# Kernel optimization log

Measured on AMD Instinct MI355X. Metric: run time of the kernel, lower is better.

The kernel has to match this reference:

```python
import jax, jax.numpy as jnp
import numpy as np

NH = 8
D_MODEL = 512
D_K = D_MODEL // NH
B, S = 2, 4096


def setup_inputs() -> dict:
    key = jax.random.key(0)
    ks = jax.random.split(key, 8)
    scale = 1.0 / np.sqrt(D_MODEL)
    return {
        "query": jax.random.normal(ks[0], (B, S, D_MODEL), dtype=jnp.float32),
        "key": jax.random.normal(ks[1], (B, S, D_MODEL), dtype=jnp.float32),
        "value": jax.random.normal(ks[2], (B, S, D_MODEL), dtype=jnp.float32),
        "mask": jax.random.randint(ks[3], (B, 1, S, S), 0, 2) > 0,
        "Wq": jax.random.normal(ks[4], (D_MODEL, D_MODEL), dtype=jnp.float32) * scale,
        "Wk": jax.random.normal(ks[5], (D_MODEL, D_MODEL), dtype=jnp.float32) * scale,
        "Wv": jax.random.normal(ks[6], (D_MODEL, D_MODEL), dtype=jnp.float32) * scale,
        "Wo": jax.random.normal(ks[7], (D_MODEL, D_MODEL), dtype=jnp.float32) * scale,
    }


def reference(query, key, value, mask, Wq, Wk, Wv, Wo):
    # Linear (no bias): torch Linear stores W as [out, in], y = x @ W^T.
    def proj(x, W):
        # [B, S, D] -> [B, nh, S, d_k]
        y = jnp.einsum("bsd,ed->bse", x, W)
        return y.reshape(B, S, NH, D_K).transpose(0, 2, 1, 3)

    q = proj(query, Wq)
    k = proj(key, Wk)
    v = proj(value, Wv)

    scores = jnp.einsum("bhqd,bhkd->bhqk", q, k) / jnp.sqrt(jnp.float32(D_K))
    scores = jnp.where(mask, jnp.float32(-1e9), scores)
    p_attn = jax.nn.softmax(scores, axis=-1)
    x = jnp.einsum("bhqk,bhkd->bhqd", p_attn, v)  # [B, nh, S, d_k]
    x = x.transpose(0, 2, 1, 3).reshape(B, S, D_MODEL)
    return jnp.einsum("bsd,ed->bse", x, Wo)
```

## Files before the change

kernel.cpp:

```cpp
#include <hip/hip_runtime.h>


#define S_LEN   4096
#define DM      512
#define NHEAD   8
#define DKH     64
#define NEG_BIG (-1e9f)
#define MINIT   (-3.402823466e38f)

typedef __bf16 bf16x8 __attribute__((ext_vector_type(8)));
typedef __bf16 bf16x4 __attribute__((ext_vector_type(4)));
typedef float  f32x4  __attribute__((ext_vector_type(4)));
typedef unsigned long long u64;

__device__ inline uint4 cvt8(float4 a, float4 b) {
    union { bf16x8 v; uint4 u; } c;
    c.v[0] = (__bf16)a.x; c.v[1] = (__bf16)a.y;
    c.v[2] = (__bf16)a.z; c.v[3] = (__bf16)a.w;
    c.v[4] = (__bf16)b.x; c.v[5] = (__bf16)b.y;
    c.v[6] = (__bf16)b.z; c.v[7] = (__bf16)b.w;
    return c.u;
}

__global__ __launch_bounds__(256)
void pack_mask(const int* __restrict__ m, u64* __restrict__ bits)
{
    const size_t i = (size_t)blockIdx.x * 256 + threadIdx.x;
    const u64 b = __ballot(m[i] != 0);
    if ((threadIdx.x & 63) == 0) bits[i >> 6] = b;
}

template<int MODE>
__global__ __launch_bounds__(512, 4)
void gemm_bf16(const void* __restrict__ Xv0, const void* __restrict__ Xv1,
               const void* __restrict__ Xv2,
               const float* __restrict__ W0, const float* __restrict__ W1,
               const float* __restrict__ W2,
               void* __restrict__ Yv0, void* __restrict__ Yv1,
               void* __restrict__ Yv2)
{
    const void* Xv; const float* W; void* Yv;
    if (blockIdx.z == 0)      { Xv = Xv0; W = W0; Yv = Yv0; }
    else if (blockIdx.z == 1) { Xv = Xv1; W = W1; Yv = Yv1; }
    else                      { Xv = Xv2; W = W2; Yv = Yv2; }
    const float oscale = (MODE == 0 && blockIdx.z == 0) ? 0.125f : 1.0f;

    __shared__ __align__(16) char lds[32768];
    char* Xs = lds;
    char* Ws = lds + 16384;

    const int tid  = threadIdx.x;
    const int lane = tid & 63;
    const int l15  = lane & 15;
    const int lhi  = lane >> 4;
    const int w    = tid >> 6;
    const int wr   = w >> 2;
    const int wc   = w & 3;
    const int row0 = blockIdx.x << 7;
    const int col0 = blockIdx.y << 7;

    const int sr = tid >> 2;
    const int sc = (tid & 3) << 1;

    f32x4 acc[4][2];
    #pragma unroll
    for (int m = 0; m < 4; ++m)
        #pragma unroll
        for (int n = 0; n < 2; ++n)
            acc[m][n] = (f32x4){0.f, 0.f, 0.f, 0.f};

    for (int k0 = 0; k0 < DM; k0 += 64) {
        uint4 xa, xb, wa, wb;
        if (MODE == 0) {
            const float* X = (const float*)Xv;
            const size_t base = (size_t)(row0 + sr) * DM + k0 + sc * 8;
            const float4 x0 = *(const float4*)&X[base];
            const float4 x1 = *(const float4*)&X[base + 4];
            const float4 x2 = *(const float4*)&X[base + 8];
            const float4 x3 = *(const float4*)&X[base + 12];
            xa = cvt8(x0, x1); xb = cvt8(x2, x3);
        } else {
            const __bf16* X = (const __bf16*)Xv;
            const size_t base = (size_t)(row0 + sr) * DM + k0 + sc * 8;
            xa = *(const uint4*)&X[base];
            xb = *(const uint4*)&X[base + 8];
        }
        {
            const size_t base = (size_t)(col0 + sr) * DM + k0 + sc * 8;
            const float4 w0_ = *(const float4*)&W[base];
            const float4 w1_ = *(const float4*)&W[base + 4];
            const float4 w2_ = *(const float4*)&W[base + 8];
            const float4 w3_ = *(const float4*)&W[base + 12];
            wa = cvt8(w0_, w1_); wb = cvt8(w2_, w3_);
        }
        __syncthreads();
        *(uint4*)(Xs + sr * 128 + ((sc       ^ (sr & 7)) << 4)) = xa;
        *(uint4*)(Xs + sr * 128 + (((sc + 1) ^ (sr & 7)) << 4)) = xb;
        *(uint4*)(Ws + sr * 128 + ((sc       ^ (sr & 7)) << 4)) = wa;
        *(uint4*)(Ws + sr * 128 + (((sc + 1) ^ (sr & 7)) << 4)) = wb;
        __syncthreads();

        #pragma unroll
        for (int kk = 0; kk < 2; ++kk) {
            bf16x8 af[4], bfr[2];
            #pragma unroll
            for (int m = 0; m < 4; ++m) {
                const int r = wr * 64 + m * 16 + l15;
                af[m] = *(const bf16x8*)(Xs + r * 128 + ((((kk << 2) + lhi) ^ (r & 7)) << 4));
            }
            #pragma unroll
            for (int n = 0; n < 2; ++n) {
                const int r = wc * 32 + n * 16 + l15;
                bfr[n] = *(const bf16x8*)(Ws + r * 128 + ((((kk << 2) + lhi) ^ (r & 7)) << 4));
            }
            #pragma unroll
            for (int m = 0; m < 4; ++m)
                #pragma unroll
                for (int n = 0; n < 2; ++n)
                    acc[m][n] = __builtin_amdgcn_mfma_f32_16x16x32_bf16(af[m], bfr[n], acc[m][n], 0, 0, 0);
        }
    }

    #pragma unroll
    for (int m = 0; m < 4; ++m) {
        #pragma unroll
        for (int n = 0; n < 2; ++n) {
            #pragma unroll
            for (int r = 0; r < 4; ++r) {
                const int row = row0 + wr * 64 + m * 16 + lhi * 4 + r;
                const int col = col0 + wc * 32 + n * 16 + l15;
                if (MODE == 0) {
                    const int b = row >> 12, srow = row & 4095;
                    const int h = col >> 6,  dk = col & 63;
                    ((__bf16*)Yv)[(((size_t)(b * NHEAD + h)) * S_LEN + srow) * DKH + dk] =
                        (__bf16)(acc[m][n][r] * oscale);
                } else {
                    ((float*)Yv)[(size_t)row * DM + col] = acc[m][n][r];
                }
            }
        }
    }
}

__global__ __launch_bounds__(512, 4)
void attn_mfma(const __bf16* __restrict__ Q, const __bf16* __restrict__ K,
               const __bf16* __restrict__ V, const u64* __restrict__ bits,
               __bf16* __restrict__ ctx)
{
    __shared__ __align__(16) char lds[32768];
    char* Ks = lds;
    char* Vt = lds + 8192;
    char* Ps = lds + 16384;

    const int tid  = threadIdx.x;
    const int lane = tid & 63;
    const int w    = tid >> 6;
    const int l15  = lane & 15;
    const int lhi  = lane >> 4;
    const int q0   = blockIdx.x << 7;
    const int h    = blockIdx.y;
    const int b    = blockIdx.z;

    const __bf16* Qb = Q + (size_t)(b * NHEAD + h) * S_LEN * DKH;
    const __bf16* Kb = K + (size_t)(b * NHEAD + h) * S_LEN * DKH;
    const __bf16* Vb = V + (size_t)(b * NHEAD + h) * S_LEN * DKH;

    const int qrow = q0 + w * 16 + l15;
    const u64* Mb = bits + (size_t)b * (S_LEN * (S_LEN / 64)) + (size_t)qrow * 64;

    const bf16x8 qa0 = *(const bf16x8*)&Qb[(size_t)qrow * DKH + lhi * 8];
    const bf16x8 qa1 = *(const bf16x8*)&Qb[(size_t)qrow * DKH + 32 + lhi * 8];

    char* psb = Ps + w * 2048;

    f32x4 o[4];
    float m_r = MINIT, l_r = 0.f;
    #pragma unroll
    for (int dt = 0; dt < 4; ++dt) o[dt] = (f32x4){0.f, 0.f, 0.f, 0.f};

    const int kj   = tid >> 3;
    const int kseg = tid & 7;
    const int vj   = tid & 63;
    const int vd0  = (tid >> 6) * 8;

    for (int kt = 0; kt < S_LEN / 64; ++kt) {
        const int j0 = kt << 6;
        const uint4 kreg = *(const uint4*)&Kb[(size_t)(j0 + kj) * DKH + kseg * 8];
        const uint4 vreg = *(const uint4*)&Vb[(size_t)(j0 + vj) * DKH + vd0];
        const u64   mw   = Mb[kt];

        __syncthreads();
        *(uint4*)(Ks + kj * 128 + ((kseg ^ (kj & 7)) << 4)) = kreg;
        {
            const __bf16* vr = (const __bf16*)&vreg;
            #pragma unroll
            for (int i = 0; i < 8; ++i) {
                const int d = vd0 + i;
                int off = d * 128 + vj * 2;
                off ^= (d & 7) << 4;
                *(__bf16*)(Vt + off) = vr[i];
            }
        }
        __syncthreads();

        f32x4 s[4];
        #pragma unroll
        for (int t = 0; t < 4; ++t) {
            const int krow = t * 16 + l15;
            const int off = krow * 128 + ((lhi ^ (krow & 7)) << 4);
            const bf16x8 kb0 = *(const bf16x8*)(Ks + off);
            const bf16x8 kb1 = *(const bf16x8*)(Ks + (off ^ 64));
            f32x4 z = (f32x4){0.f, 0.f, 0.f, 0.f};
            z = __builtin_amdgcn_mfma_f32_16x16x32_bf16(kb0, qa0, z, 0, 0, 0);
            s[t] = __builtin_amdgcn_mfma_f32_16x16x32_bf16(kb1, qa1, z, 0, 0, 0);
        }

        const unsigned int lo = (unsigned int)mw, hi = (unsigned int)(mw >> 32);
        unsigned int shf[4];
        shf[0] = lo >> (lhi << 2);
        shf[1] = lo >> (16 + (lhi << 2));
        shf[2] = hi >> (lhi << 2);
        shf[3] = hi >> (16 + (lhi << 2));

        float pv[4][4];
        #pragma unroll
        for (int t = 0; t < 4; ++t)
            #pragma unroll
            for (int r = 0; r < 4; ++r)
                pv[t][r] = ((shf[t] >> r) & 1) ? NEG_BIG : s[t][r];

        float tmax = pv[0][0];
        #pragma unroll
        for (int t = 0; t < 4; ++t)
            #pragma unroll
            for (int r = 0; r < 4; ++r)
                tmax = fmaxf(tmax, pv[t][r]);
        tmax = fmaxf(tmax, __shfl_xor(tmax, 16));
        tmax = fmaxf(tmax, __shfl_xor(tmax, 32));

        if (!__all(tmax <= m_r + 8.f)) {
            const float newm  = fmaxf(m_r, tmax);
            const float alpha = __expf(m_r - newm);
            m_r = newm;
            l_r *= alpha;
            #pragma unroll
            for (int dt = 0; dt < 4; ++dt) {
                o[dt][0] *= alpha; o[dt][1] *= alpha;
                o[dt][2] *= alpha; o[dt][3] *= alpha;
            }
        }

        float rsum = 0.f;
        #pragma unroll
        for (int t = 0; t < 4; ++t)
            #pragma unroll
            for (int r = 0; r < 4; ++r) {
                pv[t][r] = __expf(pv[t][r] - m_r);
                rsum += pv[t][r];
            }
        rsum += __shfl_xor(rsum, 16);
        rsum += __shfl_xor(rsum, 32);
        l_r += rsum;

        #pragma unroll
        for (int t = 0; t < 4; ++t)
            #pragma unroll
            for (int c = 0; c < 2; ++c) {
                union { __bf16 h2[2]; unsigned int u; } pk;
                pk.h2[0] = (__bf16)pv[t][2 * c];
                pk.h2[1] = (__bf16)pv[t][2 * c + 1];
                const int kbyte = t * 32 + (lhi << 3) + (c << 2);
                const int off = l15 * 128
                              + (((kbyte >> 4) ^ (l15 & 7)) << 4) + (kbyte & 15);
                *(unsigned int*)(psb + off) = pk.u;
            }
        const int poff = l15 * 128 + ((lhi ^ (l15 & 7)) << 4);
        const bf16x8 pb0 = *(const bf16x8*)(psb + poff);
        const bf16x8 pb1 = *(const bf16x8*)(psb + (poff ^ 64));

        #pragma unroll
        for (int dt = 0; dt < 4; ++dt) {
            const int vrow = dt * 16 + l15;
            const int voff = vrow * 128 + ((lhi ^ (vrow & 7)) << 4);
            const bf16x8 vb0 = *(const bf16x8*)(Vt + voff);
            const bf16x8 vb1 = *(const bf16x8*)(Vt + (voff ^ 64));
            o[dt] = __builtin_amdgcn_mfma_f32_16x16x32_bf16(vb0, pb0, o[dt], 0, 0, 0);
            o[dt] = __builtin_amdgcn_mfma_f32_16x16x32_bf16(vb1, pb1, o[dt], 0, 0, 0);
        }
    }

    const float inv = 1.f / l_r;
    #pragma unroll
    for (int dt = 0; dt < 4; ++dt) {
        bf16x4 ov;
        ov[0] = (__bf16)(o[dt][0] * inv);
        ov[1] = (__bf16)(o[dt][1] * inv);
        ov[2] = (__bf16)(o[dt][2] * inv);
        ov[3] = (__bf16)(o[dt][3] * inv);
        *(bf16x4*)&ctx[((size_t)b * S_LEN + qrow) * DM + h * DKH + dt * 16 + lhi * 4] = ov;
    }
}

extern "C" void kernel_launch(void* const* d_in, const int* in_sizes, int n_in,
                              void* d_out, int out_size, void* d_ws, size_t ws_size,
                              hipStream_t stream)
{
    const float* q    = (const float*)d_in[0];
    const float* k    = (const float*)d_in[1];
    const float* v    = (const float*)d_in[2];
    const int*   mask = (const int*)d_in[3];
    const float* Wq   = (const float*)d_in[4];
    const float* Wk   = (const float*)d_in[5];
    const float* Wv   = (const float*)d_in[6];
    const float* Wo   = (const float*)d_in[7];
    float* out = (float*)d_out;

    const size_t per = (size_t)2 * S_LEN * DM;
    __bf16* Qh  = (__bf16*)d_ws;
    __bf16* Kh  = Qh + per;
    __bf16* Vh  = Kh + per;
    __bf16* ctx = Vh + per;
    u64*    bits = (u64*)(ctx + per);

    pack_mask<<<dim3((2 * S_LEN * S_LEN) / 256), dim3(256), 0, stream>>>(mask, bits);

    gemm_bf16<0><<<dim3(64, 4, 3), dim3(512), 0, stream>>>(
        q, k, v, Wq, Wk, Wv, Qh, Kh, Vh);

    attn_mfma<<<dim3(S_LEN / 128, NHEAD, 2), dim3(512), 0, stream>>>(
        Qh, Kh, Vh, bits, ctx);

    gemm_bf16<1><<<dim3(64, 4, 1), dim3(512), 0, stream>>>(
        ctx, ctx, ctx, Wo, Wo, Wo, out, out, out);
}
```

Measured before the change: 436.6 us.

## Pre-cast weights, use direct-to-LDS loads, double-buffer attention K/V tiles

A new kernel casts all four weight matrices to bf16 once per call. The GEMMs then stream W, and the bf16 ctx input in the output projection, straight into LDS with global_load_lds. Epilogue stores are vectorized by swapping the MFMA operands so each lane holds contiguous columns. The attention kernel double-buffers K/V tiles in a larger LDS allocation, prefetching the next tile during compute, keeping one barrier per iteration and raising wave priority around the MFMA sections. This trades an extra small launch and higher LDS use, which may reduce occupancy, for overlap of loads with compute.

```diff
diff --git a/kernel.cpp b/kernel.cpp
--- a/kernel.cpp
+++ b/kernel.cpp
@@ -5,6 +5,7 @@
 #define DM      512
 #define NHEAD   8
 #define DKH     64
+#define NT      (S_LEN / 64)
 #define NEG_BIG (-1e9f)
 #define MINIT   (-3.402823466e38f)
 
@@ -12,6 +13,12 @@
 typedef __bf16 bf16x4 __attribute__((ext_vector_type(4)));
 typedef float  f32x4  __attribute__((ext_vector_type(4)));
 typedef unsigned long long u64;
+
+__device__ inline void gload_lds16(const void* g, void* l) {
+    __builtin_amdgcn_global_load_lds(
+        (const __attribute__((address_space(1))) unsigned int*)g,
+        (__attribute__((address_space(3))) unsigned int*)l, 16, 0, 0);
+}
 
 __device__ inline uint4 cvt8(float4 a, float4 b) {
     union { bf16x8 v; uint4 u; } c;
@@ -23,6 +30,21 @@
 }
 
 __global__ __launch_bounds__(256)
+void cast_w(const float* __restrict__ Wq, const float* __restrict__ Wk,
+            const float* __restrict__ Wv, const float* __restrict__ Wo,
+            __bf16* __restrict__ out)
+{
+    const int t = blockIdx.x * 256 + threadIdx.x;
+    const int e = t * 8;
+    const int z = e >> 18;
+    const int i = e & 262143;
+    const float* W = (z == 0) ? Wq : (z == 1) ? Wk : (z == 2) ? Wv : Wo;
+    const float4 a = *(const float4*)&W[i];
+    const float4 b = *(const float4*)&W[i + 4];
+    *(uint4*)&out[e] = cvt8(a, b);
+}
+
+__global__ __launch_bounds__(256)
 void pack_mask(const int* __restrict__ m, u64* __restrict__ bits)
 {
     const size_t i = (size_t)blockIdx.x * 256 + threadIdx.x;
@@ -32,19 +54,12 @@
 
 template<int MODE>
 __global__ __launch_bounds__(512, 4)
-void gemm_bf16(const void* __restrict__ Xv0, const void* __restrict__ Xv1,
-               const void* __restrict__ Xv2,
-               const float* __restrict__ W0, const float* __restrict__ W1,
-               const float* __restrict__ W2,
-               void* __restrict__ Yv0, void* __restrict__ Yv1,
-               void* __restrict__ Yv2)
-{
-    const void* Xv; const float* W; void* Yv;
-    if (blockIdx.z == 0)      { Xv = Xv0; W = W0; Yv = Yv0; }
-    else if (blockIdx.z == 1) { Xv = Xv1; W = W1; Yv = Yv1; }
-    else                      { Xv = Xv2; W = W2; Yv = Yv2; }
-    const float oscale = (MODE == 0 && blockIdx.z == 0) ? 0.125f : 1.0f;
-
+void gemm_mfma(const float* __restrict__ X0, const float* __restrict__ X1,
+               const float* __restrict__ X2, const __bf16* __restrict__ Xb,
+               const __bf16* __restrict__ Wb,
+               __bf16* __restrict__ Y0, __bf16* __restrict__ Y1,
+               __bf16* __restrict__ Y2, float* __restrict__ Yf)
+{
     __shared__ __align__(16) char lds[32768];
     char* Xs = lds;
     char* Ws = lds + 16384;
@@ -58,6 +73,11 @@
     const int wc   = w & 3;
     const int row0 = blockIdx.x << 7;
     const int col0 = blockIdx.y << 7;
+    const int z    = blockIdx.z;
+
+    const float*  Xf = (z == 0) ? X0 : (z == 1) ? X1 : X2;
+    __bf16*       Yb = (z == 0) ? Y0 : (z == 1) ? Y1 : Y2;
+    const __bf16* W  = Wb + (size_t)(MODE == 0 ? z : 0) * DM * DM;
 
     const int sr = tid >> 2;
     const int sc = (tid & 3) << 1;
@@ -70,73 +90,76 @@
             acc[m][n] = (f32x4){0.f, 0.f, 0.f, 0.f};
 
     for (int k0 = 0; k0 < DM; k0 += 64) {
-        uint4 xa, xb, wa, wb;
+        uint4 xa, xb2;
         if (MODE == 0) {
-            const float* X = (const float*)Xv;
             const size_t base = (size_t)(row0 + sr) * DM + k0 + sc * 8;
-            const float4 x0 = *(const float4*)&X[base];
-            const float4 x1 = *(const float4*)&X[base + 4];
-            const float4 x2 = *(const float4*)&X[base + 8];
-            const float4 x3 = *(const float4*)&X[base + 12];
-            xa = cvt8(x0, x1); xb = cvt8(x2, x3);
+            const float4 a0 = *(const float4*)&Xf[base];
+            const float4 a1 = *(const float4*)&Xf[base + 4];
+            const float4 a2 = *(const float4*)&Xf[base + 8];
+            const float4 a3 = *(const float4*)&Xf[base + 12];
+            xa = cvt8(a0, a1); xb2 = cvt8(a2, a3);
+        }
+        __syncthreads();
+        if (MODE == 0) {
+            *(uint4*)(Xs + sr * 128 + ((sc       ^ (sr & 7)) << 4)) = xa;
+            *(uint4*)(Xs + sr * 128 + (((sc + 1) ^ (sr & 7)) << 4)) = xb2;
         } else {
-            const __bf16* X = (const __bf16*)Xv;
-            const size_t base = (size_t)(row0 + sr) * DM + k0 + sc * 8;
-            xa = *(const uint4*)&X[base];
-            xb = *(const uint4*)&X[base + 8];
-        }
-        {
-            const size_t base = (size_t)(col0 + sr) * DM + k0 + sc * 8;
-            const float4 w0_ = *(const float4*)&W[base];
-            const float4 w1_ = *(const float4*)&W[base + 4];
-            const float4 w2_ = *(const float4*)&W[base + 8];
-            const float4 w3_ = *(const float4*)&W[base + 12];
-            wa = cvt8(w0_, w1_); wb = cvt8(w2_, w3_);
+            #pragma unroll
+            for (int s = 0; s < 2; ++s) {
+                const int f = w * 128 + s * 64 + lane;
+                const int r = f >> 3, sl = f & 7;
+                gload_lds16(&Xb[(size_t)(row0 + r) * DM + k0 + ((sl ^ (r & 7)) << 3)],
+                            Xs + w * 2048 + s * 1024);
+            }
+        }
+        #pragma unroll
+        for (int s = 0; s < 2; ++s) {
+            const int f = w * 128 + s * 64 + lane;
+            const int r = f >> 3, sl = f & 7;
+            gload_lds16(&W[(size_t)(col0 + r) * DM + k0 + ((sl ^ (r & 7)) << 3)],
+                        Ws + w * 2048 + s * 1024);
         }
         __syncthreads();
-        *(uint4*)(Xs + sr * 128 + ((sc       ^ (sr & 7)) << 4)) = xa;
-        *(uint4*)(Xs + sr * 128 + (((sc + 1) ^ (sr & 7)) << 4)) = xb;
-        *(uint4*)(Ws + sr * 128 + ((sc       ^ (sr & 7)) << 4)) = wa;
-        *(uint4*)(Ws + sr * 128 + (((sc + 1) ^ (sr & 7)) << 4)) = wb;
-        __syncthreads();
 
         #pragma unroll
         for (int kk = 0; kk < 2; ++kk) {
-            bf16x8 af[4], bfr[2];
+            bf16x8 xf[4], wf[2];
             #pragma unroll
             for (int m = 0; m < 4; ++m) {
                 const int r = wr * 64 + m * 16 + l15;
-                af[m] = *(const bf16x8*)(Xs + r * 128 + ((((kk << 2) + lhi) ^ (r & 7)) << 4));
+                xf[m] = *(const bf16x8*)(Xs + r * 128 + ((((kk << 2) + lhi) ^ (r & 7)) << 4));
             }
             #pragma unroll
             for (int n = 0; n < 2; ++n) {
                 const int r = wc * 32 + n * 16 + l15;
-                bfr[n] = *(const bf16x8*)(Ws + r * 128 + ((((kk << 2) + lhi) ^ (r & 7)) << 4));
+                wf[n] = *(const bf16x8*)(Ws + r * 128 + ((((kk << 2) + lhi) ^ (r & 7)) << 4));
             }
             #pragma unroll
             for (int m = 0; m < 4; ++m)
                 #pragma unroll
                 for (int n = 0; n < 2; ++n)
-                    acc[m][n] = __builtin_amdgcn_mfma_f32_16x16x32_bf16(af[m], bfr[n], acc[m][n], 0, 0, 0);
-        }
-    }
-
+                    acc[m][n] = __builtin_amdgcn_mfma_f32_16x16x32_bf16(wf[n], xf[m], acc[m][n], 0, 0, 0);
+        }
+    }
+
+    const float osc = (MODE == 0 && z == 0) ? 0.125f : 1.0f;
     #pragma unroll
     for (int m = 0; m < 4; ++m) {
+        const int r = row0 + wr * 64 + m * 16 + l15;
         #pragma unroll
         for (int n = 0; n < 2; ++n) {
-            #pragma unroll
-            for (int r = 0; r < 4; ++r) {
-                const int row = row0 + wr * 64 + m * 16 + lhi * 4 + r;
-                const int col = col0 + wc * 32 + n * 16 + l15;
-                if (MODE == 0) {
-                    const int b = row >> 12, srow = row & 4095;
-                    const int h = col >> 6,  dk = col & 63;
-                    ((__bf16*)Yv)[(((size_t)(b * NHEAD + h)) * S_LEN + srow) * DKH + dk] =
-                        (__bf16)(acc[m][n][r] * oscale);
-                } else {
-                    ((float*)Yv)[(size_t)row * DM + col] = acc[m][n][r];
-                }
+            const int cb = col0 + wc * 32 + n * 16 + lhi * 4;
+            if (MODE == 0) {
+                bf16x4 o4;
+                o4[0] = (__bf16)(acc[m][n][0] * osc);
+                o4[1] = (__bf16)(acc[m][n][1] * osc);
+                o4[2] = (__bf16)(acc[m][n][2] * osc);
+                o4[3] = (__bf16)(acc[m][n][3] * osc);
+                const int bb = r >> 12, srow = r & 4095;
+                const int hh = cb >> 6, dk = cb & 63;
+                *(bf16x4*)&Yb[(((size_t)(bb * NHEAD + hh)) * S_LEN + srow) * DKH + dk] = o4;
+            } else {
+                *(float4*)&Yf[(size_t)r * DM + cb] = *(float4*)&acc[m][n];
             }
         }
     }
@@ -147,10 +170,7 @@
                const __bf16* __restrict__ V, const u64* __restrict__ bits,
                __bf16* __restrict__ ctx)
 {
-    __shared__ __align__(16) char lds[32768];
-    char* Ks = lds;
-    char* Vt = lds + 8192;
-    char* Ps = lds + 16384;
+    __shared__ __align__(16) char lds[49152];
 
     const int tid  = threadIdx.x;
     const int lane = tid & 63;
@@ -171,51 +191,58 @@
     const bf16x8 qa0 = *(const bf16x8*)&Qb[(size_t)qrow * DKH + lhi * 8];
     const bf16x8 qa1 = *(const bf16x8*)&Qb[(size_t)qrow * DKH + 32 + lhi * 8];
 
-    char* psb = Ps + w * 2048;
+    char* psb = lds + 32768 + w * 2048;
 
     f32x4 o[4];
     float m_r = MINIT, l_r = 0.f;
     #pragma unroll
     for (int dt = 0; dt < 4; ++dt) o[dt] = (f32x4){0.f, 0.f, 0.f, 0.f};
 
-    const int kj   = tid >> 3;
-    const int kseg = tid & 7;
-    const int vj   = tid & 63;
-    const int vd0  = (tid >> 6) * 8;
-
-    for (int kt = 0; kt < S_LEN / 64; ++kt) {
-        const int j0 = kt << 6;
-        const uint4 kreg = *(const uint4*)&Kb[(size_t)(j0 + kj) * DKH + kseg * 8];
-        const uint4 vreg = *(const uint4*)&Vb[(size_t)(j0 + vj) * DKH + vd0];
-        const u64   mw   = Mb[kt];
-
-        __syncthreads();
-        *(uint4*)(Ks + kj * 128 + ((kseg ^ (kj & 7)) << 4)) = kreg;
-        {
-            const __bf16* vr = (const __bf16*)&vreg;
-            #pragma unroll
-            for (int i = 0; i < 8; ++i) {
-                const int d = vd0 + i;
-                int off = d * 128 + vj * 2;
-                off ^= (d & 7) << 4;
-                *(__bf16*)(Vt + off) = vr[i];
-            }
-        }
-        __syncthreads();
+    const int krow = tid >> 3, kslot = tid & 7;
+    const int vj   = tid & 63, vd0 = (tid >> 6) * 8;
+
+    gload_lds16(&Kb[(size_t)krow * DKH + ((kslot ^ (krow & 7)) << 3)],
+                lds + w * 1024);
+    {
+        const uint4 v0 = *(const uint4*)&Vb[(size_t)vj * DKH + vd0];
+        char* Vt = lds + 8192;
+        const __bf16* vr = (const __bf16*)&v0;
+        #pragma unroll
+        for (int i = 0; i < 8; ++i) {
+            const int d = vd0 + i;
+            *(__bf16*)(Vt + ((d * 128 + vj * 2) ^ ((d & 7) << 4))) = vr[i];
+        }
+    }
+    u64 mcur = Mb[0];
+    __syncthreads();
+
+    for (int t = 0; t < NT; ++t) {
+        const int c  = t & 1;
+        const int tn = (t + 1 < NT) ? (t + 1) : t;
+
+        gload_lds16(&Kb[(size_t)((tn << 6) + krow) * DKH + ((kslot ^ (krow & 7)) << 3)],
+                    lds + (c ^ 1) * 16384 + w * 1024);
+        const uint4 vnxt = *(const uint4*)&Vb[(size_t)((tn << 6) + vj) * DKH + vd0];
+        const u64   mnxt = Mb[tn];
+
+        const char* Ksb = lds + c * 16384;
+        const char* Vtb = Ksb + 8192;
 
         f32x4 s[4];
-        #pragma unroll
-        for (int t = 0; t < 4; ++t) {
-            const int krow = t * 16 + l15;
-            const int off = krow * 128 + ((lhi ^ (krow & 7)) << 4);
-            const bf16x8 kb0 = *(const bf16x8*)(Ks + off);
-            const bf16x8 kb1 = *(const bf16x8*)(Ks + (off ^ 64));
-            f32x4 z = (f32x4){0.f, 0.f, 0.f, 0.f};
-            z = __builtin_amdgcn_mfma_f32_16x16x32_bf16(kb0, qa0, z, 0, 0, 0);
-            s[t] = __builtin_amdgcn_mfma_f32_16x16x32_bf16(kb1, qa1, z, 0, 0, 0);
-        }
-
-        const unsigned int lo = (unsigned int)mw, hi = (unsigned int)(mw >> 32);
+        __builtin_amdgcn_s_setprio(1);
+        #pragma unroll
+        for (int tt = 0; tt < 4; ++tt) {
+            const int kr  = tt * 16 + l15;
+            const int off = kr * 128 + ((lhi ^ (kr & 7)) << 4);
+            const bf16x8 kb0 = *(const bf16x8*)(Ksb + off);
+            const bf16x8 kb1 = *(const bf16x8*)(Ksb + (off ^ 64));
+            f32x4 zz = (f32x4){0.f, 0.f, 0.f, 0.f};
+            zz    = __builtin_amdgcn_mfma_f32_16x16x32_bf16(kb0, qa0, zz, 0, 0, 0);
+            s[tt] = __builtin_amdgcn_mfma_f32_16x16x32_bf16(kb1, qa1, zz, 0, 0, 0);
+        }
+        __builtin_amdgcn_s_setprio(0);
+
+        const unsigned int lo = (unsigned int)mcur, hi = (unsigned int)(mcur >> 32);
         unsigned int shf[4];
         shf[0] = lo >> (lhi << 2);
         shf[1] = lo >> (16 + (lhi << 2));
@@ -224,17 +251,17 @@
 
         float pv[4][4];
         #pragma unroll
-        for (int t = 0; t < 4; ++t)
+        for (int tt = 0; tt < 4; ++tt)
             #pragma unroll
             for (int r = 0; r < 4; ++r)
-                pv[t][r] = ((shf[t] >> r) & 1) ? NEG_BIG : s[t][r];
+                pv[tt][r] = ((shf[tt] >> r) & 1) ? NEG_BIG : s[tt][r];
 
         float tmax = pv[0][0];
         #pragma unroll
-        for (int t = 0; t < 4; ++t)
+        for (int tt = 0; tt < 4; ++tt)
             #pragma unroll
             for (int r = 0; r < 4; ++r)
-                tmax = fmaxf(tmax, pv[t][r]);
+                tmax = fmaxf(tmax, pv[tt][r]);
         tmax = fmaxf(tmax, __shfl_xor(tmax, 16));
         tmax = fmaxf(tmax, __shfl_xor(tmax, 32));
 
@@ -252,24 +279,24 @@
 
         float rsum = 0.f;
         #pragma unroll
-        for (int t = 0; t < 4; ++t)
+        for (int tt = 0; tt < 4; ++tt)
             #pragma unroll
             for (int r = 0; r < 4; ++r) {
-                pv[t][r] = __expf(pv[t][r] - m_r);
-                rsum += pv[t][r];
+                pv[tt][r] = __expf(pv[tt][r] - m_r);
+                rsum += pv[tt][r];
             }
         rsum += __shfl_xor(rsum, 16);
         rsum += __shfl_xor(rsum, 32);
         l_r += rsum;
 
         #pragma unroll
-        for (int t = 0; t < 4; ++t)
-            #pragma unroll
-            for (int c = 0; c < 2; ++c) {
+        for (int tt = 0; tt < 4; ++tt)
+            #pragma unroll
+            for (int cc = 0; cc < 2; ++cc) {
                 union { __bf16 h2[2]; unsigned int u; } pk;
-                pk.h2[0] = (__bf16)pv[t][2 * c];
-                pk.h2[1] = (__bf16)pv[t][2 * c + 1];
-                const int kbyte = t * 32 + (lhi << 3) + (c << 2);
+                pk.h2[0] = (__bf16)pv[tt][2 * cc];
+                pk.h2[1] = (__bf16)pv[tt][2 * cc + 1];
+                const int kbyte = tt * 32 + (lhi << 3) + (cc << 2);
                 const int off = l15 * 128
                               + (((kbyte >> 4) ^ (l15 & 7)) << 4) + (kbyte & 15);
                 *(unsigned int*)(psb + off) = pk.u;
@@ -278,15 +305,29 @@
         const bf16x8 pb0 = *(const bf16x8*)(psb + poff);
         const bf16x8 pb1 = *(const bf16x8*)(psb + (poff ^ 64));
 
+        __builtin_amdgcn_s_setprio(1);
         #pragma unroll
         for (int dt = 0; dt < 4; ++dt) {
             const int vrow = dt * 16 + l15;
             const int voff = vrow * 128 + ((lhi ^ (vrow & 7)) << 4);
-            const bf16x8 vb0 = *(const bf16x8*)(Vt + voff);
-            const bf16x8 vb1 = *(const bf16x8*)(Vt + (voff ^ 64));
+            const bf16x8 vb0 = *(const bf16x8*)(Vtb + voff);
+            const bf16x8 vb1 = *(const bf16x8*)(Vtb + (voff ^ 64));
             o[dt] = __builtin_amdgcn_mfma_f32_16x16x32_bf16(vb0, pb0, o[dt], 0, 0, 0);
             o[dt] = __builtin_amdgcn_mfma_f32_16x16x32_bf16(vb1, pb1, o[dt], 0, 0, 0);
         }
+        __builtin_amdgcn_s_setprio(0);
+
+        {
+            char* Vt = lds + (c ^ 1) * 16384 + 8192;
+            const __bf16* vr = (const __bf16*)&vnxt;
+            #pragma unroll
+            for (int i = 0; i < 8; ++i) {
+                const int d = vd0 + i;
+                *(__bf16*)(Vt + ((d * 128 + vj * 2) ^ ((d & 7) << 4))) = vr[i];
+            }
+        }
+        __syncthreads();
+        mcur = mnxt;
     }
 
     const float inv = 1.f / l_r;
@@ -316,20 +357,24 @@
     float* out = (float*)d_out;
 
     const size_t per = (size_t)2 * S_LEN * DM;
-    __bf16* Qh  = (__bf16*)d_ws;
-    __bf16* Kh  = Qh + per;
-    __bf16* Vh  = Kh + per;
-    __bf16* ctx = Vh + per;
+    __bf16* wb   = (__bf16*)d_ws;
+    __bf16* Qh   = wb + (size_t)4 * DM * DM;
+    __bf16* Kh   = Qh + per;
+    __bf16* Vh   = Kh + per;
+    __bf16* ctx  = Vh + per;
     u64*    bits = (u64*)(ctx + per);
 
+    cast_w<<<dim3(512), dim3(256), 0, stream>>>(Wq, Wk, Wv, Wo, wb);
+
     pack_mask<<<dim3((2 * S_LEN * S_LEN) / 256), dim3(256), 0, stream>>>(mask, bits);
 
-    gemm_bf16<0><<<dim3(64, 4, 3), dim3(512), 0, stream>>>(
-        q, k, v, Wq, Wk, Wv, Qh, Kh, Vh);
+    gemm_mfma<0><<<dim3(64, 4, 3), dim3(512), 0, stream>>>(
+        q, k, v, nullptr, wb, Qh, Kh, Vh, nullptr);
 
     attn_mfma<<<dim3(S_LEN / 128, NHEAD, 2), dim3(512), 0, stream>>>(
         Qh, Kh, Vh, bits, ctx);
 
-    gemm_bf16<1><<<dim3(64, 4, 1), dim3(512), 0, stream>>>(
-        ctx, ctx, ctx, Wo, Wo, Wo, out, out, out);
-}
+    gemm_mfma<1><<<dim3(64, 4, 1), dim3(512), 0, stream>>>(
+        nullptr, nullptr, nullptr, ctx, wb + (size_t)3 * DM * DM,
+        nullptr, nullptr, nullptr, out);
+}
```

Measured after the change: 420.4 us. -3.7%, faster.
